# Kernel optimization log

Measured on AMD Instinct MI355X. Metric: run time of the kernel, lower is better.

## Reference

```python
import jax, jax.numpy as jnp
import numpy as np

B, T, H, L, O = 64, 256, 1024, 4, 1024
LN_EPS = 1e-5


def setup_inputs() -> dict:
    key = jax.random.key(0)
    ks = jax.random.split(key, 8)
    s = 1.0 / np.sqrt(H)
    return {
        "inputs": jax.random.normal(ks[0], (B, T, H), jnp.float32),
        "Wx": jax.random.normal(ks[1], (L, H, H), jnp.float32) * s,   # torch Linear weight [out,in]
        "bx": jax.random.normal(ks[2], (L, H), jnp.float32) * s,
        "Wh": jax.random.normal(ks[3], (L, H, H), jnp.float32) * s,   # bias=False
        "ln_g": jnp.ones((L, H), jnp.float32),
        "ln_b": jnp.zeros((L, H), jnp.float32),
        "Wy": jax.random.normal(ks[4], (O, H), jnp.float32) * s,
        "by": jax.random.normal(ks[5], (O,), jnp.float32) * s,
    }


def _layernorm(z, g, b):
    mu = jnp.mean(z, axis=-1, keepdims=True)
    var = jnp.mean(jnp.square(z - mu), axis=-1, keepdims=True)
    return (z - mu) * jax.lax.rsqrt(var + LN_EPS) * g + b


def _forward(inputs, Wx, bx, Wh, ln_g, ln_b, Wy, by):
    x = inputs                                  # [B, T, H]
    n_layers = Wx.shape[0]
    for l in range(n_layers):
        Wx_l, bx_l, Wh_l = Wx[l], bx[l], Wh[l]
        g_l, b_l = ln_g[l], ln_b[l]

        def step(h, x_t):
            # h_t = tanh(LN(x_t Wx^T + bx + h Wh^T))  (dropout off in eval)
            z = x_t @ Wx_l.T + bx_l + h @ Wh_l.T
            h_new = jnp.tanh(_layernorm(z, g_l, b_l))
            return h_new, h_new

        h0 = jnp.zeros((x.shape[0], Wh_l.shape[0]), x.dtype)
        _, hs = jax.lax.scan(step, h0, jnp.swapaxes(x, 0, 1))  # hs: [T, B, H]
        x = jnp.swapaxes(hs, 0, 1)                              # [B, T, H]
    y = x @ Wy.T + by                                           # [B, T, O]
    return x, y


def reference(inputs, Wx, bx, Wh, ln_g, ln_b, Wy, by):
    return _forward(inputs, Wx, bx, Wh, ln_g, ln_b, Wy, by)
```

## Files before the change

### kernel.cpp

```cpp
#include <hip/hip_runtime.h>
#include <stdint.h>

#define B_ 64
#define T_ 256
#define H_ 1024
#define L_ 4
#define O_ 1024
#define LN_EPS 1e-5f
#define RING 4

typedef short v8s __attribute__((ext_vector_type(8)));
typedef float v4f __attribute__((ext_vector_type(4)));
typedef unsigned long long u64t;

__device__ __forceinline__ unsigned short f2bf(float f) {
  union { float f; unsigned u; } v; v.f = f;
  unsigned r = (v.u + 0x7FFFu + ((v.u >> 16) & 1u)) >> 16;
  return (unsigned short)r;
}
__device__ __forceinline__ float bf2f(unsigned short u) {
  union { unsigned u; float f; } v; v.u = ((unsigned)u) << 16; return v.f;
}
__device__ __forceinline__ float tanh_fast(float x) {
  float e = __expf(2.0f * x);
  return 1.0f - 2.0f / (e + 1.0f);
}

__device__ __forceinline__ int hswz(int row, int kq) {
  return ((row << 7) + ((kq ^ (kq >> 4) ^ row) & 127)) << 3;
}

__device__ __forceinline__ void poll_ge(const int* p, int v) {
  int it = 0;
  while (__hip_atomic_load(p, __ATOMIC_RELAXED, __HIP_MEMORY_SCOPE_AGENT) < v) {
    __builtin_amdgcn_s_sleep(1);
    if (++it > (1 << 20)) break;
  }
}

__global__ void k_f2b(const float* __restrict__ src, unsigned short* __restrict__ dst, int n4) {
  int i = blockIdx.x * blockDim.x + threadIdx.x;
  int stride = gridDim.x * blockDim.x;
  for (; i < n4; i += stride) {
    float4 v = *(const float4*)(src + 4 * (size_t)i);
    union { unsigned short u[4]; uint2 q; } p;
    p.u[0] = f2bf(v.x); p.u[1] = f2bf(v.y); p.u[2] = f2bf(v.z); p.u[3] = f2bf(v.w);
    *(uint2*)(dst + 4 * (size_t)i) = p.q;
  }
}

__launch_bounds__(256, 2)
__global__ void k_gemm(const unsigned short* __restrict__ Xb,
                       const unsigned short* __restrict__ Wb,
                       const float* __restrict__ bias,
                       float* __restrict__ Cout, int swap_rows) {
  __shared__ short As[128][40];
  __shared__ short Bs[128][40];
  int bm = blockIdx.x >> 3, bn = blockIdx.x & 7;
  int row0 = bm * 128, col0 = bn * 128;
  int tid = threadIdx.x, lane = tid & 63, w = tid >> 6;
  int wm = w >> 1, wn = w & 1;
  int m15 = lane & 15, quad = lane >> 4;
  v4f acc[4][4];
  #pragma unroll
  for (int a = 0; a < 4; ++a)
    #pragma unroll
    for (int b = 0; b < 4; ++b) acc[a][b] = (v4f){0.f, 0.f, 0.f, 0.f};

  int srow = tid >> 1, sseg = tid & 1;
  const unsigned short* gA = Xb + (size_t)(row0 + srow) * 1024 + sseg * 16;
  const unsigned short* gB = Wb + (size_t)(col0 + srow) * 1024 + sseg * 16;

  for (int kb = 0; kb < 32; ++kb) {
    v8s a0 = *(const v8s*)(gA + kb * 32);
    v8s a1 = *(const v8s*)(gA + kb * 32 + 8);
    v8s b0 = *(const v8s*)(gB + kb * 32);
    v8s b1 = *(const v8s*)(gB + kb * 32 + 8);
    *(v8s*)&As[srow][sseg * 16]     = a0;
    *(v8s*)&As[srow][sseg * 16 + 8] = a1;
    *(v8s*)&Bs[srow][sseg * 16]     = b0;
    *(v8s*)&Bs[srow][sseg * 16 + 8] = b1;
    __syncthreads();
    v8s af[4], bfr[4];
    #pragma unroll
    for (int mt = 0; mt < 4; ++mt) af[mt]  = *(v8s*)&As[wm * 64 + mt * 16 + m15][quad * 8];
    #pragma unroll
    for (int nt = 0; nt < 4; ++nt) bfr[nt] = *(v8s*)&Bs[wn * 64 + nt * 16 + m15][quad * 8];
    #pragma unroll
    for (int mt = 0; mt < 4; ++mt)
      #pragma unroll
      for (int nt = 0; nt < 4; ++nt)
        acc[mt][nt] = __builtin_amdgcn_mfma_f32_16x16x32_bf16(af[mt], bfr[nt], acc[mt][nt], 0, 0, 0);
    __syncthreads();
  }
  #pragma unroll
  for (int mt = 0; mt < 4; ++mt) {
    #pragma unroll
    for (int nt = 0; nt < 4; ++nt) {
      int col = col0 + wn * 64 + nt * 16 + m15;
      float bv = bias[col];
      #pragma unroll
      for (int r = 0; r < 4; ++r) {
        int row = row0 + wm * 64 + mt * 16 + quad * 4 + r;
        int orow = swap_rows ? ((row & 63) * 256 + (row >> 6)) : row;
        Cout[(size_t)orow * 1024 + col] = acc[mt][nt][r] + bv;
      }
    }
  }
}

__launch_bounds__(256, 1)
__global__ void k_fused(const float* __restrict__ inp,
                        const unsigned short* __restrict__ Whb_all,
                        const unsigned short* __restrict__ Wxb_all,
                        const float* __restrict__ bx_all,
                        const float* __restrict__ lng_all,
                        const float* __restrict__ lnb_all,
                        unsigned short* Xbuf,
                        float* Zr,
                        int* flags,
                        float* __restrict__ outx)
{
  __shared__ short hs[16 * 1024];
  __shared__ short xs[16 * 1024];
  __shared__ float sG[1024], sB[1024];

  const int tid = threadIdx.x, lane = tid & 63, w = tid >> 6;
  const int bid = blockIdx.x;
  const int l = bid >> 6, rb = (bid >> 4) & 3, cb = bid & 15;
  const int r0 = rb * 16, c0 = cb * 64;
  const int m15 = lane & 15, quad = lane >> 4;
  const int myrow = 4 * w + quad;
  const int chunk = m15;

  for (int i = tid; i < 1024; i += 256) { sG[i] = lng_all[l * H_ + i]; sB[i] = lnb_all[l * H_ + i]; }

  v8s bh[32], bx8[32];
  {
    const unsigned short* wr = Whb_all + ((size_t)l * H_ + c0 + w * 16 + m15) * H_ + quad * 8;
    #pragma unroll
    for (int ks = 0; ks < 32; ++ks) bh[ks] = *(const v8s*)(wr + ks * 32);
    const unsigned short* wx = Wxb_all + ((size_t)l * H_ + c0 + w * 16 + m15) * H_ + quad * 8;
    #pragma unroll
    for (int ks = 0; ks < 32; ++ks) bx8[ks] = *(const v8s*)(wx + ks * 32);
  }

  const float bias = bx_all[l * H_ + c0 + w * 16 + m15];
  int* myfz = flags + ((l * 64 + rb * 16 + cb) << 5);
  const int* peer_fz = flags + ((l * 64 + rb * 16 + chunk) << 5);
  const int* prev_fz = (l > 0) ? flags + (((l - 1) * 64 + rb * 16 + chunk) << 5) : (const int*)nullptr;

  const size_t TBH = (size_t)T_ * B_ * H_;
  unsigned short* Xout = Xbuf + (size_t)l * TBH;
  const unsigned short* Xin = (l > 0) ? Xbuf + (size_t)(l - 1) * TBH : (const unsigned short*)nullptr;
  float* Zl = Zr + (size_t)l * RING * 4 * 16 * 1024;

  auto stage_x = [&](int t1) {
    if (l == 0) {
      const float* src = inp + ((size_t)(r0 + myrow) * T_ + t1) * H_ + chunk * 64;
      #pragma unroll
      for (int g8 = 0; g8 < 8; ++g8) {
        float4 q0 = *(const float4*)(src + g8 * 8);
        float4 q1 = *(const float4*)(src + g8 * 8 + 4);
        v8s hp;
        hp[0] = (short)f2bf(q0.x); hp[1] = (short)f2bf(q0.y);
        hp[2] = (short)f2bf(q0.z); hp[3] = (short)f2bf(q0.w);
        hp[4] = (short)f2bf(q1.x); hp[5] = (short)f2bf(q1.y);
        hp[6] = (short)f2bf(q1.z); hp[7] = (short)f2bf(q1.w);
        *(v8s*)&xs[hswz(myrow, chunk * 8 + g8)] = hp;
      }
    } else {
      const unsigned short* src = Xin + ((size_t)t1 * B_ + r0 + myrow) * H_ + chunk * 64;
      #pragma unroll
      for (int g8 = 0; g8 < 8; ++g8)
        *(v8s*)&xs[hswz(myrow, chunk * 8 + g8)] = *(const v8s*)(src + g8 * 8);
    }
  };

  if (l > 0) poll_ge(prev_fz, 2);
  stage_x(0);
  __syncthreads();
  v4f acc = (v4f){bias, bias, bias, bias};
  #pragma unroll
  for (int ks = 0; ks < 32; ++ks) {
    v8s a = *(const v8s*)&xs[hswz(m15, ks * 4 + quad)];
    acc = __builtin_amdgcn_mfma_f32_16x16x32_bf16(a, bx8[ks], acc, 0, 0, 0);
  }

  for (int t = 0; t < T_; ++t) {
    float* zo = Zl + (size_t)((t & (RING - 1)) * 4 + rb) * 16 * 1024;
    #pragma unroll
    for (int r = 0; r < 4; ++r)
      __hip_atomic_store(&zo[(size_t)(quad * 4 + r) * H_ + c0 + w * 16 + m15], acc[r],
                         __ATOMIC_RELAXED, __HIP_MEMORY_SCOPE_AGENT);
    __syncthreads();
    if (tid == 0)
      __hip_atomic_store(myfz, t + 1, __ATOMIC_RELAXED, __HIP_MEMORY_SCOPE_AGENT);

    if (t < T_ - 1) {
      if (l > 0) poll_ge(prev_fz, t + 3);
      stage_x(t + 1);
      __syncthreads();
      acc = (v4f){bias, bias, bias, bias};
      #pragma unroll
      for (int ks = 0; ks < 32; ++ks) {
        v8s a = *(const v8s*)&xs[hswz(m15, ks * 4 + quad)];
        acc = __builtin_amdgcn_mfma_f32_16x16x32_bf16(a, bx8[ks], acc, 0, 0, 0);
      }
    }

    poll_ge(peer_fz, t + 1);
    const u64t* zp = (const u64t*)(zo + (size_t)myrow * H_ + chunk * 64);
    float2 zr2[32];
    #pragma unroll
    for (int j = 0; j < 32; ++j) {
      union { u64t u; float2 f; } cv;
      cv.u = __hip_atomic_load(zp + j, __ATOMIC_RELAXED, __HIP_MEMORY_SCOPE_AGENT);
      zr2[j] = cv.f;
    }
    float s = 0.f, s2 = 0.f;
    #pragma unroll
    for (int j = 0; j < 32; ++j) {
      s  += zr2[j].x + zr2[j].y;
      s2 += zr2[j].x * zr2[j].x + zr2[j].y * zr2[j].y;
    }
    #pragma unroll
    for (int m = 1; m < 16; m <<= 1) { s += __shfl_xor(s, m); s2 += __shfl_xor(s2, m); }
    float mu = s * (1.f / 1024.f);
    float var = s2 * (1.f / 1024.f) - mu * mu;
    float rs = rsqrtf(var + LN_EPS);
    #pragma unroll
    for (int g8 = 0; g8 < 8; ++g8) {
      v8s hp;
      #pragma unroll
      for (int e = 0; e < 8; ++e) {
        int colg = chunk * 64 + g8 * 8 + e;
        float zv = (e & 1) ? zr2[g8 * 4 + (e >> 1)].y : zr2[g8 * 4 + (e >> 1)].x;
        float hv = tanh_fast((zv - mu) * rs * sG[colg] + sB[colg]);
        hp[e] = (short)f2bf(hv);
      }
      *(v8s*)&hs[hswz(myrow, chunk * 8 + g8)] = hp;
    }
    __syncthreads();

    {
      int row = tid >> 4, ci = tid & 15;
      int colbase = c0 + ci * 4;
      const short* hp = &hs[hswz(row, colbase >> 3) + (ci & 1) * 4];
      union { unsigned short u[4]; u64t q; } pk;
      pk.u[0] = (unsigned short)hp[0]; pk.u[1] = (unsigned short)hp[1];
      pk.u[2] = (unsigned short)hp[2]; pk.u[3] = (unsigned short)hp[3];
      u64t* xdst = (u64t*)(Xout + ((size_t)t * B_ + r0 + row) * H_ + colbase);
      if (l < L_ - 1) {
        __hip_atomic_store(xdst, pk.q, __ATOMIC_RELAXED, __HIP_MEMORY_SCOPE_AGENT);
      } else {
        *xdst = pk.q;
        float4 f;
        f.x = bf2f(pk.u[0]); f.y = bf2f(pk.u[1]); f.z = bf2f(pk.u[2]); f.w = bf2f(pk.u[3]);
        *(float4*)(outx + ((size_t)(r0 + row) * T_ + t) * H_ + colbase) = f;
      }
    }
    if (t < T_ - 1) {
      #pragma unroll
      for (int ks = 0; ks < 32; ++ks) {
        v8s a = *(const v8s*)&hs[hswz(m15, ks * 4 + quad)];
        acc = __builtin_amdgcn_mfma_f32_16x16x32_bf16(a, bh[ks], acc, 0, 0, 0);
      }
    }
  }
  __syncthreads();
  if (tid == 0)
    __hip_atomic_store(myfz, T_ + 1, __ATOMIC_RELAXED, __HIP_MEMORY_SCOPE_AGENT);
}

extern "C" void kernel_launch(void* const* d_in, const int* in_sizes, int n_in,
                              void* d_out, int out_size, void* d_ws, size_t ws_size,
                              hipStream_t stream) {
  const float* inp = (const float*)d_in[0];
  const float* Wx  = (const float*)d_in[1];
  const float* bx  = (const float*)d_in[2];
  const float* Wh  = (const float*)d_in[3];
  const float* lng = (const float*)d_in[4];
  const float* lnb = (const float*)d_in[5];
  const float* Wy  = (const float*)d_in[6];
  const float* by  = (const float*)d_in[7];
  float* out_x = (float*)d_out;
  float* out_y = out_x + (size_t)B_ * T_ * H_;

  char* ws = (char*)d_ws;
  unsigned short* Whb  = (unsigned short*)(ws);
  unsigned short* Wxb  = (unsigned short*)(ws + ((size_t)8 << 20));
  unsigned short* Wyb  = (unsigned short*)(ws + ((size_t)16 << 20));
  int* flags           = (int*)(ws + ((size_t)18 << 20));
  float* Zr            = (float*)(ws + ((size_t)19 << 20));
  unsigned short* Xbuf = (unsigned short*)(ws + ((size_t)23 << 20));

  hipMemsetAsync(flags, 0, (size_t)L_ * 64 * 32 * sizeof(int), stream);
  k_f2b<<<1024, 256, 0, stream>>>(Wh, Whb, (L_ * H_ * H_) / 4);
  k_f2b<<<1024, 256, 0, stream>>>(Wx, Wxb, (L_ * H_ * H_) / 4);
  k_f2b<<<256, 256, 0, stream>>>(Wy, Wyb, (O_ * H_) / 4);

  k_fused<<<L_ * 64, 256, 0, stream>>>(inp, Whb, Wxb, bx, lng, lnb,
                                       Xbuf, Zr, flags, out_x);

  k_gemm<<<1024, 256, 0, stream>>>(Xbuf + (size_t)(L_ - 1) * T_ * B_ * H_,
                                   Wyb, by, out_y, 1);
}
```

Baseline: 4.581 ms.

## Stream Wx fragments from global, pre-transpose input, read output GEMM from fp32 x

Layer-0 input is converted to bf16 and transposed to time-major in a separate prep kernel, so the fused recurrent kernel reads x_t straight from global memory instead of staging it through shared memory. The Wx register fragments are dropped and streamed from global/L2 each step, cutting register pressure and the xs shared buffer. The last layer no longer writes a bf16 copy; the output projection GEMM reads the fp32 outx and converts on the fly. This trades register and LDS use for extra global and L2 traffic on the per-step input projection, which sits on the serial critical path.

Measured after the change: 5.175 ms. 1.13x slower.

```diff
diff --git a/kernel.cpp b/kernel.cpp
--- a/kernel.cpp
+++ b/kernel.cpp
@@ -7,7 +7,8 @@
 #define L_ 4
 #define O_ 1024
 #define LN_EPS 1e-5f
-#define RING 4
+#define RING_Z 4
+#define POLL_CAP (1 << 20)
 
 typedef short v8s __attribute__((ext_vector_type(8)));
 typedef float v4f __attribute__((ext_vector_type(4)));
@@ -34,7 +35,7 @@
   int it = 0;
   while (__hip_atomic_load(p, __ATOMIC_RELAXED, __HIP_MEMORY_SCOPE_AGENT) < v) {
     __builtin_amdgcn_s_sleep(1);
-    if (++it > (1 << 20)) break;
+    if (++it > POLL_CAP) break;
   }
 }
 
@@ -49,11 +50,24 @@
   }
 }
 
+__global__ void k_prep_x(const float* __restrict__ in, unsigned short* __restrict__ X) {
+  int row = blockIdx.x;
+  int b = row >> 8, t = row & 255;
+  const float* src = in + (size_t)row * H_;
+  unsigned short* dst = X + ((size_t)t * B_ + b) * H_;
+  for (int j = threadIdx.x; j < H_ / 4; j += blockDim.x) {
+    float4 v = *(const float4*)(src + 4 * j);
+    union { unsigned short u[4]; uint2 q; } p;
+    p.u[0] = f2bf(v.x); p.u[1] = f2bf(v.y); p.u[2] = f2bf(v.z); p.u[3] = f2bf(v.w);
+    *(uint2*)(dst + 4 * j) = p.q;
+  }
+}
+
 __launch_bounds__(256, 2)
-__global__ void k_gemm(const unsigned short* __restrict__ Xb,
-                       const unsigned short* __restrict__ Wb,
-                       const float* __restrict__ bias,
-                       float* __restrict__ Cout, int swap_rows) {
+__global__ void k_gemm32(const float* __restrict__ Xf,
+                         const unsigned short* __restrict__ Wb,
+                         const float* __restrict__ bias,
+                         float* __restrict__ Cout) {
   __shared__ short As[128][40];
   __shared__ short Bs[128][40];
   int bm = blockIdx.x >> 3, bn = blockIdx.x & 7;
@@ -68,12 +82,19 @@
     for (int b = 0; b < 4; ++b) acc[a][b] = (v4f){0.f, 0.f, 0.f, 0.f};
 
   int srow = tid >> 1, sseg = tid & 1;
-  const unsigned short* gA = Xb + (size_t)(row0 + srow) * 1024 + sseg * 16;
+  const float* gA = Xf + (size_t)(row0 + srow) * 1024 + sseg * 16;
   const unsigned short* gB = Wb + (size_t)(col0 + srow) * 1024 + sseg * 16;
 
   for (int kb = 0; kb < 32; ++kb) {
-    v8s a0 = *(const v8s*)(gA + kb * 32);
-    v8s a1 = *(const v8s*)(gA + kb * 32 + 8);
+    float4 f0 = *(const float4*)(gA + kb * 32);
+    float4 f1 = *(const float4*)(gA + kb * 32 + 4);
+    float4 f2 = *(const float4*)(gA + kb * 32 + 8);
+    float4 f3 = *(const float4*)(gA + kb * 32 + 12);
+    v8s a0, a1;
+    a0[0] = (short)f2bf(f0.x); a0[1] = (short)f2bf(f0.y); a0[2] = (short)f2bf(f0.z); a0[3] = (short)f2bf(f0.w);
+    a0[4] = (short)f2bf(f1.x); a0[5] = (short)f2bf(f1.y); a0[6] = (short)f2bf(f1.z); a0[7] = (short)f2bf(f1.w);
+    a1[0] = (short)f2bf(f2.x); a1[1] = (short)f2bf(f2.y); a1[2] = (short)f2bf(f2.z); a1[3] = (short)f2bf(f2.w);
+    a1[4] = (short)f2bf(f3.x); a1[5] = (short)f2bf(f3.y); a1[6] = (short)f2bf(f3.z); a1[7] = (short)f2bf(f3.w);
     v8s b0 = *(const v8s*)(gB + kb * 32);
     v8s b1 = *(const v8s*)(gB + kb * 32 + 8);
     *(v8s*)&As[srow][sseg * 16]     = a0;
@@ -102,27 +123,24 @@
       #pragma unroll
       for (int r = 0; r < 4; ++r) {
         int row = row0 + wm * 64 + mt * 16 + quad * 4 + r;
-        int orow = swap_rows ? ((row & 63) * 256 + (row >> 6)) : row;
-        Cout[(size_t)orow * 1024 + col] = acc[mt][nt][r] + bv;
+        Cout[(size_t)row * 1024 + col] = acc[mt][nt][r] + bv;
       }
     }
   }
 }
 
 __launch_bounds__(256, 1)
-__global__ void k_fused(const float* __restrict__ inp,
-                        const unsigned short* __restrict__ Whb_all,
+__global__ void k_fused(const unsigned short* __restrict__ Whb_all,
                         const unsigned short* __restrict__ Wxb_all,
                         const float* __restrict__ bx_all,
                         const float* __restrict__ lng_all,
                         const float* __restrict__ lnb_all,
-                        unsigned short* Xbuf,
+                        unsigned short* Xl,
                         float* Zr,
-                        int* flags,
+                        int* fz,
                         float* __restrict__ outx)
 {
   __shared__ short hs[16 * 1024];
-  __shared__ short xs[16 * 1024];
   __shared__ float sG[1024], sB[1024];
 
   const int tid = threadIdx.x, lane = tid & 63, w = tid >> 6;
@@ -132,66 +150,50 @@
   const int m15 = lane & 15, quad = lane >> 4;
   const int myrow = 4 * w + quad;
   const int chunk = m15;
+  const int colg = c0 + w * 16 + m15;
 
   for (int i = tid; i < 1024; i += 256) { sG[i] = lng_all[l * H_ + i]; sB[i] = lnb_all[l * H_ + i]; }
 
-  v8s bh[32], bx8[32];
+  v8s bh[32];
   {
-    const unsigned short* wr = Whb_all + ((size_t)l * H_ + c0 + w * 16 + m15) * H_ + quad * 8;
+    const unsigned short* wr = Whb_all + ((size_t)l * H_ + colg) * H_ + quad * 8;
     #pragma unroll
     for (int ks = 0; ks < 32; ++ks) bh[ks] = *(const v8s*)(wr + ks * 32);
-    const unsigned short* wx = Wxb_all + ((size_t)l * H_ + c0 + w * 16 + m15) * H_ + quad * 8;
-    #pragma unroll
-    for (int ks = 0; ks < 32; ++ks) bx8[ks] = *(const v8s*)(wx + ks * 32);
-  }
-
-  const float bias = bx_all[l * H_ + c0 + w * 16 + m15];
-  int* myfz = flags + ((l * 64 + rb * 16 + cb) << 5);
-  const int* peer_fz = flags + ((l * 64 + rb * 16 + chunk) << 5);
-  const int* prev_fz = (l > 0) ? flags + (((l - 1) * 64 + rb * 16 + chunk) << 5) : (const int*)nullptr;
+  }
+
+  const float bias = bx_all[l * H_ + colg];
+  const unsigned short* wxb = Wxb_all + ((size_t)l * H_ + colg) * H_ + quad * 8;
+  int* myfz = fz + ((l * 64 + rb * 16 + cb) << 5);
+  const int* peer_fz = fz + ((l * 64 + rb * 16 + chunk) << 5);
+  const int* prev_fz = (l > 0) ? fz + (((l - 1) * 64 + rb * 16 + chunk) << 5) : (const int*)nullptr;
 
   const size_t TBH = (size_t)T_ * B_ * H_;
-  unsigned short* Xout = Xbuf + (size_t)l * TBH;
-  const unsigned short* Xin = (l > 0) ? Xbuf + (size_t)(l - 1) * TBH : (const unsigned short*)nullptr;
-  float* Zl = Zr + (size_t)l * RING * 4 * 16 * 1024;
-
-  auto stage_x = [&](int t1) {
-    if (l == 0) {
-      const float* src = inp + ((size_t)(r0 + myrow) * T_ + t1) * H_ + chunk * 64;
-      #pragma unroll
-      for (int g8 = 0; g8 < 8; ++g8) {
-        float4 q0 = *(const float4*)(src + g8 * 8);
-        float4 q1 = *(const float4*)(src + g8 * 8 + 4);
-        v8s hp;
-        hp[0] = (short)f2bf(q0.x); hp[1] = (short)f2bf(q0.y);
-        hp[2] = (short)f2bf(q0.z); hp[3] = (short)f2bf(q0.w);
-        hp[4] = (short)f2bf(q1.x); hp[5] = (short)f2bf(q1.y);
-        hp[6] = (short)f2bf(q1.z); hp[7] = (short)f2bf(q1.w);
-        *(v8s*)&xs[hswz(myrow, chunk * 8 + g8)] = hp;
-      }
-    } else {
-      const unsigned short* src = Xin + ((size_t)t1 * B_ + r0 + myrow) * H_ + chunk * 64;
-      #pragma unroll
-      for (int g8 = 0; g8 < 8; ++g8)
-        *(v8s*)&xs[hswz(myrow, chunk * 8 + g8)] = *(const v8s*)(src + g8 * 8);
-    }
-  };
+  const unsigned short* Xin = Xl + (size_t)l * TBH;
+  unsigned short* Xout = (l < L_ - 1) ? Xl + (size_t)(l + 1) * TBH : (unsigned short*)nullptr;
+  float* Zl = Zr + (size_t)l * RING_Z * 4 * 16 * 1024;
 
   if (l > 0) poll_ge(prev_fz, 2);
-  stage_x(0);
   __syncthreads();
   v4f acc = (v4f){bias, bias, bias, bias};
-  #pragma unroll
-  for (int ks = 0; ks < 32; ++ks) {
-    v8s a = *(const v8s*)&xs[hswz(m15, ks * 4 + quad)];
-    acc = __builtin_amdgcn_mfma_f32_16x16x32_bf16(a, bx8[ks], acc, 0, 0, 0);
+  {
+    const unsigned short* xr = Xin + ((size_t)r0 + m15) * H_ + quad * 8;
+    #pragma unroll 1
+    for (int kb = 0; kb < 4; ++kb) {
+      #pragma unroll
+      for (int k8 = 0; k8 < 8; ++k8) {
+        int ks = kb * 8 + k8;
+        v8s a = *(const v8s*)(xr + ks * 32);
+        v8s b = *(const v8s*)(wxb + ks * 32);
+        acc = __builtin_amdgcn_mfma_f32_16x16x32_bf16(a, b, acc, 0, 0, 0);
+      }
+    }
   }
 
   for (int t = 0; t < T_; ++t) {
-    float* zo = Zl + (size_t)((t & (RING - 1)) * 4 + rb) * 16 * 1024;
+    float* zo = Zl + (size_t)((t & (RING_Z - 1)) * 4 + rb) * 16 * 1024;
     #pragma unroll
     for (int r = 0; r < 4; ++r)
-      __hip_atomic_store(&zo[(size_t)(quad * 4 + r) * H_ + c0 + w * 16 + m15], acc[r],
+      __hip_atomic_store(&zo[(size_t)(quad * 4 + r) * H_ + colg], acc[r],
                          __ATOMIC_RELAXED, __HIP_MEMORY_SCOPE_AGENT);
     __syncthreads();
     if (tid == 0)
@@ -199,13 +201,18 @@
 
     if (t < T_ - 1) {
       if (l > 0) poll_ge(prev_fz, t + 3);
-      stage_x(t + 1);
       __syncthreads();
       acc = (v4f){bias, bias, bias, bias};
-      #pragma unroll
-      for (int ks = 0; ks < 32; ++ks) {
-        v8s a = *(const v8s*)&xs[hswz(m15, ks * 4 + quad)];
-        acc = __builtin_amdgcn_mfma_f32_16x16x32_bf16(a, bx8[ks], acc, 0, 0, 0);
+      const unsigned short* xr = Xin + ((size_t)(t + 1) * B_ + r0 + m15) * H_ + quad * 8;
+      #pragma unroll 1
+      for (int kb = 0; kb < 4; ++kb) {
+        #pragma unroll
+        for (int k8 = 0; k8 < 8; ++k8) {
+          int ks = kb * 8 + k8;
+          v8s a = *(const v8s*)(xr + ks * 32);
+          v8s b = *(const v8s*)(wxb + ks * 32);
+          acc = __builtin_amdgcn_mfma_f32_16x16x32_bf16(a, b, acc, 0, 0, 0);
+        }
       }
     }
 
@@ -234,9 +241,9 @@
       v8s hp;
       #pragma unroll
       for (int e = 0; e < 8; ++e) {
-        int colg = chunk * 64 + g8 * 8 + e;
+        int cg = chunk * 64 + g8 * 8 + e;
         float zv = (e & 1) ? zr2[g8 * 4 + (e >> 1)].y : zr2[g8 * 4 + (e >> 1)].x;
-        float hv = tanh_fast((zv - mu) * rs * sG[colg] + sB[colg]);
+        float hv = tanh_fast((zv - mu) * rs * sG[cg] + sB[cg]);
         hp[e] = (short)f2bf(hv);
       }
       *(v8s*)&hs[hswz(myrow, chunk * 8 + g8)] = hp;
@@ -250,11 +257,10 @@
       union { unsigned short u[4]; u64t q; } pk;
       pk.u[0] = (unsigned short)hp[0]; pk.u[1] = (unsigned short)hp[1];
       pk.u[2] = (unsigned short)hp[2]; pk.u[3] = (unsigned short)hp[3];
-      u64t* xdst = (u64t*)(Xout + ((size_t)t * B_ + r0 + row) * H_ + colbase);
       if (l < L_ - 1) {
+        u64t* xdst = (u64t*)(Xout + ((size_t)t * B_ + r0 + row) * H_ + colbase);
         __hip_atomic_store(xdst, pk.q, __ATOMIC_RELAXED, __HIP_MEMORY_SCOPE_AGENT);
       } else {
-        *xdst = pk.q;
         float4 f;
         f.x = bf2f(pk.u[0]); f.y = bf2f(pk.u[1]); f.z = bf2f(pk.u[2]); f.w = bf2f(pk.u[3]);
         *(float4*)(outx + ((size_t)(r0 + row) * T_ + t) * H_ + colbase) = f;
@@ -288,21 +294,20 @@
   float* out_y = out_x + (size_t)B_ * T_ * H_;
 
   char* ws = (char*)d_ws;
-  unsigned short* Whb  = (unsigned short*)(ws);
-  unsigned short* Wxb  = (unsigned short*)(ws + ((size_t)8 << 20));
-  unsigned short* Wyb  = (unsigned short*)(ws + ((size_t)16 << 20));
-  int* flags           = (int*)(ws + ((size_t)18 << 20));
-  float* Zr            = (float*)(ws + ((size_t)19 << 20));
-  unsigned short* Xbuf = (unsigned short*)(ws + ((size_t)23 << 20));
-
-  hipMemsetAsync(flags, 0, (size_t)L_ * 64 * 32 * sizeof(int), stream);
+  unsigned short* Whb = (unsigned short*)(ws);
+  unsigned short* Wxb = (unsigned short*)(ws + ((size_t)8 << 20));
+  unsigned short* Wyb = (unsigned short*)(ws + ((size_t)16 << 20));
+  int* fzf            = (int*)(ws + ((size_t)18 << 20));
+  float* Zr           = (float*)(ws + ((size_t)19 << 20));
+  unsigned short* Xl  = (unsigned short*)(ws + ((size_t)23 << 20));
+
+  hipMemsetAsync(fzf, 0, (size_t)L_ * 64 * 32 * sizeof(int), stream);
   k_f2b<<<1024, 256, 0, stream>>>(Wh, Whb, (L_ * H_ * H_) / 4);
   k_f2b<<<1024, 256, 0, stream>>>(Wx, Wxb, (L_ * H_ * H_) / 4);
   k_f2b<<<256, 256, 0, stream>>>(Wy, Wyb, (O_ * H_) / 4);
-
-  k_fused<<<L_ * 64, 256, 0, stream>>>(inp, Whb, Wxb, bx, lng, lnb,
-                                       Xbuf, Zr, flags, out_x);
-
-  k_gemm<<<1024, 256, 0, stream>>>(Xbuf + (size_t)(L_ - 1) * T_ * B_ * H_,
-                                   Wyb, by, out_y, 1);
-}
+  k_prep_x<<<B_ * T_, 256, 0, stream>>>(inp, Xl);
+
+  k_fused<<<256, 256, 0, stream>>>(Whb, Wxb, bx, lng, lnb, Xl, Zr, fzf, out_x);
+
+  k_gemm32<<<1024, 256, 0, stream>>>(out_x, Wyb, by, out_y);
+}
```
